# Kernel optimization log

Hardware: AMD Instinct MI355X
Metric: run time of the kernel (lower is better)

## Reference

```python
import jax, jax.numpy as jnp
import numpy as np

B, D, H = 131072, 1024, 128
ALL_PERMS = jnp.array([[0, 1, 2], [0, 2, 1], [1, 0, 2],
                       [1, 2, 0], [2, 0, 1], [2, 1, 0]], dtype=jnp.int32)


def setup_inputs() -> dict:
    key = jax.random.key(0)
    ks = jax.random.split(key, 10)
    inp_dim = D + 12  # d_model + 9 (state) + 3 (round one-hot)
    seq_embed = jax.random.normal(ks[0], (B, D), jnp.float32)
    freq = jax.random.uniform(ks[1], (B, 3), jnp.float32)
    pres = (jax.random.uniform(ks[2], (B, 3)) < 0.5).astype(jnp.float32)
    round_mask = (jax.random.uniform(ks[3], (B, 3)) < 0.5).astype(jnp.float32)
    perm_idx = jax.random.randint(ks[4], (B,), 0, 6, jnp.int32)
    W1 = jax.random.normal(ks[5], (inp_dim, H), jnp.float32) / np.sqrt(inp_dim).astype(np.float32)
    b1 = jnp.zeros((H,), jnp.float32)
    W2 = jax.random.normal(ks[6], (H, H), jnp.float32) / np.sqrt(H).astype(np.float32)
    b2 = jnp.zeros((H,), jnp.float32)
    W3 = jax.random.normal(ks[7], (H, 2), jnp.float32) / np.sqrt(H).astype(np.float32)
    b3 = jnp.zeros((2,), jnp.float32)
    return {"seq_embed": seq_embed, "freq": freq, "pres": pres,
            "round_mask": round_mask, "perm_idx": perm_idx,
            "W1": W1, "b1": b1, "W2": W2, "b2": b2, "W3": W3, "b3": b3}


def reference(seq_embed, freq, pres, round_mask, perm_idx, W1, b1, W2, b2, W3, b3):
    b = seq_embed.shape[0]
    dt = seq_embed.dtype
    perms = ALL_PERMS[perm_idx]                      # [B,3] round order per sample
    state = jnp.zeros((b, 9), dt)                    # 3 slots x [freq, pres, decoded]
    dec_f = jnp.zeros((b, 3), dt)
    dec_p = jnp.zeros((b, 3), dt)
    loss_sum = jnp.zeros((), dt)
    n_masked = jnp.zeros((), dt)
    ones_b = jnp.ones((b,), dt)
    for step in range(3):                            # fixed 3-step unroll (as original)
        ridx = perms[:, step]                        # [B]
        oh = jax.nn.one_hot(ridx, 3, dtype=dt)       # [B,3]
        gt_f = jnp.sum(freq * oh, axis=1)            # gather via one-hot
        gt_p = jnp.sum(pres * oh, axis=1)
        m = jnp.sum(round_mask * oh, axis=1)
        inp = jnp.concatenate([seq_embed, state, oh], axis=1)  # [B, D+12]
        h = jax.nn.gelu(inp @ W1 + b1, approximate=False)
        h = jax.nn.gelu(h @ W2 + b2, approximate=False)
        pred = h @ W3 + b3                           # [B,2]
        pf, z = pred[:, 0], pred[:, 1]
        fl = jnp.square(pf - gt_f) * m
        # sigmoid_cross_entropy_with_logits, numerically stable
        pl = (jnp.maximum(z, 0.0) - z * gt_p + jnp.log1p(jnp.exp(-jnp.abs(z)))) * m
        loss_sum = loss_sum + jnp.sum(fl + pl)
        n_masked = n_masked + jnp.sum(m)
        act_f = jnp.where(m > 0.5, pf, gt_f)
        act_p = jnp.where(m > 0.5, jax.nn.sigmoid(z), gt_p)
        new_vals = jnp.stack([act_f, act_p, ones_b], axis=1)   # [B,3]
        # scatter new_vals into slot ridx of state
        state3 = state.reshape(b, 3, 3)
        state = (state3 * (1.0 - oh)[:, :, None]
                 + new_vals[:, None, :] * oh[:, :, None]).reshape(b, 9)
        dec_f = dec_f * (1.0 - oh) + act_f[:, None] * oh
        dec_p = dec_p * (1.0 - oh) + act_p[:, None] * oh
    autoreg_loss = loss_sum / (n_masked + 1e-8)
    return autoreg_loss, dec_f, dec_p
```

## Files before the change

### kernel.cpp

```cpp
#include <hip/hip_runtime.h>
#include <math.h>

#define DDIM 1024
#define HDIM 128
#define BK 32

typedef float  f32x4  __attribute__((ext_vector_type(4)));
typedef __bf16 bf16x8 __attribute__((ext_vector_type(8)));

union BF2U { __bf16 h; ushort u; };

__constant__ int c_perms[6][3] = {{0,1,2},{0,2,1},{1,0,2},{1,2,0},{2,0,1},{2,1,0}};

__device__ __forceinline__ ushort f2bf(float f){
    BF2U c; c.h = (__bf16)f; return c.u;
}
__device__ __forceinline__ float gelu_fast(float x){
    float a = fabsf(x) * 0.70710678118654752f;
    float t = __frcp_rn(fmaf(0.3275911f, a, 1.0f));
    float p = t * fmaf(t, fmaf(t, fmaf(t, fmaf(t, 1.061405429f, -1.453152027f),
                 1.421413741f), -0.284496736f), 0.254829592f);
    float y = 1.0f - p * __expf(-a * a);
    float er = copysignf(y, x);
    return 0.5f * x * (1.0f + er);
}

__global__ __launch_bounds__(256) void k0_prep(const float* __restrict__ W1,
                                               const float* __restrict__ W2,
                                               ushort* __restrict__ w1s,
                                               ushort* __restrict__ w2t)
{
    int i = blockIdx.x * 256 + threadIdx.x;
    if (i < DDIM * HDIM) {
        int t = i >> 12, rem = i & 4095;
        int n = rem >> 5, kk = rem & 31;
        int k = t * 32 + kk;
        w1s[i] = f2bf(W1[(size_t)k * HDIM + n]);
    } else if (i < DDIM * HDIM + HDIM * HDIM) {
        int j = i - DDIM * HDIM;
        int k = j >> 7, n = j & 127;
        ushort b = f2bf(W2[(size_t)k * HDIM + n]);
        size_t off = (size_t)n * 256 + (size_t)(((k * 2) ^ ((n & 7) << 4)));
        w2t[off >> 1] = b;
    }
}

__global__ __launch_bounds__(256, 2) void kf_fused(
    const float* __restrict__ seq,
    const ushort* __restrict__ w1s,
    const ushort* __restrict__ w2t,
    const float* __restrict__ freq,
    const float* __restrict__ pres,
    const float* __restrict__ rmask,
    const int*   __restrict__ pidx,
    const float* __restrict__ W1,
    const float* __restrict__ b1,
    const float* __restrict__ b2,
    const float* __restrict__ W3,
    const float* __restrict__ b3,
    float* __restrict__ dec_f,
    float* __restrict__ dec_p,
    float* __restrict__ partials)
{
    __shared__ __align__(16) char lds[73728];
    const int t = threadIdx.x;
    const int wid = t >> 6, lane = t & 63;
    const int g = lane >> 4, ln = lane & 15;
    const size_t row0 = (size_t)blockIdx.x * 128;

    char* const As0 = lds;
    char* const Bs0 = lds + 49152;

    const int srow = wid * 8 + (lane >> 3);
    const int scolb = ((lane & 7) * 16) ^ ((lane >> 3) << 4);
    const int sldsw = wid * 1024;
    const int blane = lane * 16;

#define STAGE(BUF, TT) do { \
    _Pragma("unroll") \
    for (int j_ = 0; j_ < 4; ++j_) { \
        const char* ga_ = (const char*)(seq + (row0 + j_ * 32 + srow) * DDIM + (TT) * BK) + scolb; \
        char* la_ = As0 + (BUF) * 16384 + j_ * 4096 + sldsw; \
        __builtin_amdgcn_global_load_lds((const __attribute__((address_space(1))) void*)ga_, \
                                         (__attribute__((address_space(3))) void*)la_, 16, 0, 0); \
    } \
    _Pragma("unroll") \
    for (int i_ = 0; i_ < 2; ++i_) { \
        const char* gb_ = (const char*)w1s + (size_t)(TT) * 8192 + i_ * 4096 + sldsw + blane; \
        char* lb_ = Bs0 + (BUF) * 8192 + i_ * 4096 + sldsw; \
        __builtin_amdgcn_global_load_lds((const __attribute__((address_space(1))) void*)gb_, \
                                         (__attribute__((address_space(3))) void*)lb_, 16, 0, 0); \
    } } while (0)

#define COMPUTE(BUF) do { \
    bf16x8 af[2]; \
    _Pragma("unroll") \
    for (int mf = 0; mf < 2; ++mf) { \
        const int row = wid * 32 + mf * 16 + ln; \
        const int sw = (row & 7) << 4; \
        f32x4 x0 = *reinterpret_cast<const f32x4*>(As0 + (BUF) * 16384 + row * 128 + ((g * 32 +  0) ^ sw)); \
        f32x4 x1 = *reinterpret_cast<const f32x4*>(As0 + (BUF) * 16384 + row * 128 + ((g * 32 + 16) ^ sw)); \
        af[mf][0] = (__bf16)x0[0]; af[mf][1] = (__bf16)x0[1]; \
        af[mf][2] = (__bf16)x0[2]; af[mf][3] = (__bf16)x0[3]; \
        af[mf][4] = (__bf16)x1[0]; af[mf][5] = (__bf16)x1[1]; \
        af[mf][6] = (__bf16)x1[2]; af[mf][7] = (__bf16)x1[3]; \
    } \
    const ushort* btile = reinterpret_cast<const ushort*>(Bs0 + (BUF) * 8192); \
    _Pragma("unroll") \
    for (int nf = 0; nf < 8; ++nf) { \
        bf16x8 bb = *reinterpret_cast<const bf16x8*>(btile + nf * 512 + ln * 32 + g * 8); \
        acc[0][nf] = __builtin_amdgcn_mfma_f32_16x16x32_bf16(af[0], bb, acc[0][nf], 0, 0, 0); \
        acc[1][nf] = __builtin_amdgcn_mfma_f32_16x16x32_bf16(af[1], bb, acc[1][nf], 0, 0, 0); \
    } } while (0)

#define WAITBAR(N) do { \
    asm volatile("s_waitcnt vmcnt(" #N ")" ::: "memory"); \
    __builtin_amdgcn_sched_barrier(0); \
    __builtin_amdgcn_s_barrier(); \
    __builtin_amdgcn_sched_barrier(0); } while (0)

    f32x4 acc[2][8];
#pragma unroll
    for (int m = 0; m < 2; ++m)
#pragma unroll
        for (int n = 0; n < 8; ++n) acc[m][n] = (f32x4){0.f, 0.f, 0.f, 0.f};

    STAGE(0, 0);
    STAGE(1, 1);
    int cur = 0, nxt2 = 2;
    for (int tt = 0; tt < 30; ++tt) {
        WAITBAR(6);
        STAGE(nxt2, tt + 2);
        COMPUTE(cur);
        cur  = (cur  == 2) ? 0 : cur  + 1;
        nxt2 = (nxt2 == 2) ? 0 : nxt2 + 1;
    }
    WAITBAR(6);
    COMPUTE(cur);
    cur = (cur == 2) ? 0 : cur + 1;
    WAITBAR(0);
    COMPUTE(cur);
#undef WAITBAR
#undef COMPUTE
#undef STAGE

    __syncthreads();

    {
        float b1v[8];
#pragma unroll
        for (int nf = 0; nf < 8; ++nf) b1v[nf] = b1[nf * 16 + ln];
#pragma unroll
        for (int mf = 0; mf < 2; ++mf)
#pragma unroll
            for (int nf = 0; nf < 8; ++nf)
#pragma unroll
                for (int r = 0; r < 4; ++r) {
                    int row = wid * 32 + mf * 16 + g * 4 + r;
                    int colb = (nf * 32 + ln * 2) ^ ((row & 7) << 4);
                    *reinterpret_cast<ushort*>(lds + row * 256 + colb) = f2bf(acc[mf][nf][r] + b1v[nf]);
                }
    }
#pragma unroll
    for (int i = 0; i < 8; ++i) {
        const char* gs = (const char*)w2t + wid * 8192 + i * 1024 + blane;
        char* ds = lds + 32768 + wid * 8192 + i * 1024;
        __builtin_amdgcn_global_load_lds((const __attribute__((address_space(1))) void*)gs,
                                         (__attribute__((address_space(3))) void*)ds, 16, 0, 0);
    }
    {
        float* W1es = (float*)(lds + 65536);
        for (int i = t; i < 12 * 128; i += 256)
            W1es[i] = W1[(size_t)(DDIM + (i >> 7)) * HDIM + (i & 127)];
    }
    __syncthreads();

    const char*  W2s  = lds + 32768;
    const float* W1es = (const float*)(lds + 65536);
    float* stl  = (float*)(lds + 71680);
    float* redl = (float*)(lds + 72192);

    float b2v[8], w30[8], w31[8];
#pragma unroll
    for (int nf = 0; nf < 8; ++nf) {
        b2v[nf] = b2[nf * 16 + ln];
        w30[nf] = W3[(nf * 16 + ln) * 2 + 0];
        w31[nf] = W3[(nf * 16 + ln) * 2 + 1];
    }
    const float b30 = b3[0], b31 = b3[1];
    const bool owner = (ln < 4);
    float lossAcc = 0.f, maskAcc = 0.f;

    for (int p = 0; p < 2; ++p) {
        const int rowLocal = wid * 16 + ln;
        const int ctRow = p * 64 + rowLocal;
        const size_t R_h = row0 + ctRow;
        const int pidx_h = pidx[R_h];

        float scon[32];
        {
            const int swzr = (rowLocal & 7) << 4;
#pragma unroll
            for (int ks = 0; ks < 4; ++ks) {
                bf16x8 v = *reinterpret_cast<const bf16x8*>(lds + ctRow * 256 + ((ks * 64 + g * 16) ^ swzr));
#pragma unroll
                for (int j = 0; j < 8; ++j) scon[ks * 8 + j] = (float)v[j];
            }
        }
        const int rloc_own = wid * 16 + g * 4 + ln;
        const size_t R_own = row0 + (size_t)p * 64 + rloc_own;
        int pio = 0;
        float ffo[3] = {0,0,0}, ppo[3] = {0,0,0}, mmo[3] = {0,0,0};
        if (owner) {
            pio = pidx[R_own];
#pragma unroll
            for (int q = 0; q < 3; ++q) {
                ffo[q] = freq[R_own * 3 + q];
                ppo[q] = pres[R_own * 3 + q];
                mmo[q] = rmask[R_own * 3 + q];
            }
        }

        for (int s = 0; s < 3; ++s) {
            const int ridx_h = c_perms[pidx_h][s];
            bf16x8 afr[4];
#pragma unroll
            for (int ks = 0; ks < 4; ++ks) {
                const float* ohp = &W1es[(9 + ridx_h) * 128 + ks * 32 + g * 8];
                f32x4 o0 = *reinterpret_cast<const f32x4*>(ohp);
                f32x4 o1 = *reinterpret_cast<const f32x4*>(ohp + 4);
#pragma unroll
                for (int j = 0; j < 4; ++j) {
                    afr[ks][j]     = (__bf16)gelu_fast(scon[ks * 8 + j]     + o0[j]);
                    afr[ks][4 + j] = (__bf16)gelu_fast(scon[ks * 8 + 4 + j] + o1[j]);
                }
            }
            f32x4 acc2[8];
#pragma unroll
            for (int nf = 0; nf < 8; ++nf) acc2[nf] = (f32x4){0.f, 0.f, 0.f, 0.f};
#pragma unroll
            for (int ks = 0; ks < 4; ++ks) {
#pragma unroll
                for (int nf = 0; nf < 8; ++nf) {
                    const int n = nf * 16 + ln;
                    bf16x8 bb = *reinterpret_cast<const bf16x8*>(W2s + n * 256 + ((ks * 64 + g * 16) ^ ((n & 7) << 4)));
                    acc2[nf] = __builtin_amdgcn_mfma_f32_16x16x32_bf16(afr[ks], bb, acc2[nf], 0, 0, 0);
                }
            }
            float p0[4] = {0, 0, 0, 0}, p1[4] = {0, 0, 0, 0};
#pragma unroll
            for (int nf = 0; nf < 8; ++nf) {
#pragma unroll
                for (int r = 0; r < 4; ++r) {
                    float h2 = gelu_fast(acc2[nf][r] + b2v[nf]);
                    p0[r] += h2 * w30[nf];
                    p1[r] += h2 * w31[nf];
                }
            }
#pragma unroll
            for (int mk = 1; mk < 16; mk <<= 1) {
#pragma unroll
                for (int r = 0; r < 4; ++r) {
                    p0[r] += __shfl_xor(p0[r], mk);
                    p1[r] += __shfl_xor(p1[r], mk);
                }
            }
            if (owner) {
                const int ridx_o = c_perms[pio][s];
                float pf = ((ln == 0) ? p0[0] : (ln == 1) ? p0[1] : (ln == 2) ? p0[2] : p0[3]) + b30;
                float z  = ((ln == 0) ? p1[0] : (ln == 1) ? p1[1] : (ln == 2) ? p1[2] : p1[3]) + b31;
                float gt_f = (ridx_o == 0) ? ffo[0] : (ridx_o == 1) ? ffo[1] : ffo[2];
                float gt_p = (ridx_o == 0) ? ppo[0] : (ridx_o == 1) ? ppo[1] : ppo[2];
                float m    = (ridx_o == 0) ? mmo[0] : (ridx_o == 1) ? mmo[1] : mmo[2];
                float d = pf - gt_f;
                float pl = (fmaxf(z, 0.f) - z * gt_p + __logf(1.0f + __expf(-fabsf(z)))) * m;
                lossAcc += d * d * m + pl;
                maskAcc += m;
                bool msk = m > 0.5f;
                float act_f = msk ? pf : gt_f;
                float act_p = msk ? (1.f / (1.f + __expf(-z))) : gt_p;
                stl[rloc_own * 2 + 0] = act_f;
                stl[rloc_own * 2 + 1] = act_p;
                dec_f[R_own * 3 + ridx_o] = act_f;
                dec_p[R_own * 3 + ridx_o] = act_p;
            }
            if (s < 2) {
                float af = stl[rowLocal * 2 + 0];
                float ap = stl[rowLocal * 2 + 1];
                const float* w0r = &W1es[(ridx_h * 3 + 0) * 128];
                const float* w1r = &W1es[(ridx_h * 3 + 1) * 128];
                const float* w2r = &W1es[(ridx_h * 3 + 2) * 128];
#pragma unroll
                for (int ks = 0; ks < 4; ++ks) {
                    const int c0 = ks * 32 + g * 8;
                    f32x4 a0 = *reinterpret_cast<const f32x4*>(w0r + c0);
                    f32x4 a1 = *reinterpret_cast<const f32x4*>(w0r + c0 + 4);
                    f32x4 b0 = *reinterpret_cast<const f32x4*>(w1r + c0);
                    f32x4 b1x = *reinterpret_cast<const f32x4*>(w1r + c0 + 4);
                    f32x4 c0v = *reinterpret_cast<const f32x4*>(w2r + c0);
                    f32x4 c1v = *reinterpret_cast<const f32x4*>(w2r + c0 + 4);
#pragma unroll
                    for (int j = 0; j < 4; ++j) {
                        scon[ks * 8 + j]     += af * a0[j] + ap * b0[j]  + c0v[j];
                        scon[ks * 8 + 4 + j] += af * a1[j] + ap * b1x[j] + c1v[j];
                    }
                }
            }
        }
    }
#pragma unroll
    for (int mk = 1; mk < 64; mk <<= 1) {
        lossAcc += __shfl_xor(lossAcc, mk);
        maskAcc += __shfl_xor(maskAcc, mk);
    }
    if (lane == 0) { redl[wid * 2] = lossAcc; redl[wid * 2 + 1] = maskAcc; }
    __syncthreads();
    if (t == 0) {
        float ls = 0.f, ms = 0.f;
#pragma unroll
        for (int w = 0; w < 4; ++w) { ls += redl[w * 2]; ms += redl[w * 2 + 1]; }
        partials[2 * (size_t)blockIdx.x]     = ls;
        partials[2 * (size_t)blockIdx.x + 1] = ms;
    }
}

__global__ __launch_bounds__(256) void k3_reduce(const float* __restrict__ partials,
                                                 int nb, float* __restrict__ out)
{
    __shared__ float sl[256], sm[256];
    int t = threadIdx.x;
    float ls = 0.f, ms = 0.f;
    for (int i = t; i < nb; i += 256) { ls += partials[2 * i]; ms += partials[2 * i + 1]; }
    sl[t] = ls; sm[t] = ms;
    __syncthreads();
    for (int s = 128; s > 0; s >>= 1) {
        if (t < s) { sl[t] += sl[t + s]; sm[t] += sm[t + s]; }
        __syncthreads();
    }
    if (t == 0) out[0] = sl[0] / (sm[0] + 1e-8f);
}

extern "C" void kernel_launch(void* const* d_in, const int* in_sizes, int n_in,
                              void* d_out, int out_size, void* d_ws, size_t ws_size,
                              hipStream_t stream) {
    const float* seq   = (const float*)d_in[0];
    const float* freq  = (const float*)d_in[1];
    const float* pres  = (const float*)d_in[2];
    const float* rmask = (const float*)d_in[3];
    const int*   pidx  = (const int*)d_in[4];
    const float* W1    = (const float*)d_in[5];
    const float* b1    = (const float*)d_in[6];
    const float* W2    = (const float*)d_in[7];
    const float* b2    = (const float*)d_in[8];
    const float* W3    = (const float*)d_in[9];
    const float* b3    = (const float*)d_in[10];

    int B = in_sizes[4];
    float* out   = (float*)d_out;
    float* dec_f = out + 1;
    float* dec_p = out + 1 + (size_t)B * 3;

    char* ws = (char*)d_ws;
    float*  partials = (float*)ws;
    ushort* w1s  = (ushort*)(ws + 16384);
    ushort* w2t  = (ushort*)(ws + 16384 + 262144);

    int nblk = B / 128;
    k0_prep<<<(DDIM * HDIM + HDIM * HDIM + 255) / 256, 256, 0, stream>>>(W1, W2, w1s, w2t);
    kf_fused<<<nblk, 256, 0, stream>>>(seq, w1s, w2t, freq, pres, rmask, pidx,
                                       W1, b1, b2, W3, b3, dec_f, dec_p, partials);
    k3_reduce<<<1, 256, 0, stream>>>(partials, nblk, out);
}
```

Measured before the change: 202.4 us.

## Make each wave own its rows and drop block barriers from the GEMM loop

Restructures the fused MLP kernel so each wave stages and processes its own 32 rows in a private LDS arena, removing the per-iteration block barrier from the layer-1 K loop. W1 tiles now go directly from global memory into registers, triple-buffered across iterations, instead of through LDS. W2 is preloaded into LDS once at kernel start. The small W1 extra rows are read from global memory rather than copied into LDS. This raises register pressure and global reads of W1 per wave, and the LDS footprint grows.

```diff
diff --git a/kernel.cpp b/kernel.cpp
--- a/kernel.cpp
+++ b/kernel.cpp
@@ -3,7 +3,6 @@
 
 #define DDIM 1024
 #define HDIM 128
-#define BK 32
 
 typedef float  f32x4  __attribute__((ext_vector_type(4)));
 typedef __bf16 bf16x8 __attribute__((ext_vector_type(8)));
@@ -62,61 +61,64 @@
     float* __restrict__ dec_p,
     float* __restrict__ partials)
 {
-    __shared__ __align__(16) char lds[73728];
+    __shared__ __align__(16) char lds[81920];
     const int t = threadIdx.x;
     const int wid = t >> 6, lane = t & 63;
     const int g = lane >> 4, ln = lane & 15;
-    const size_t row0 = (size_t)blockIdx.x * 128;
-
-    char* const As0 = lds;
-    char* const Bs0 = lds + 49152;
-
-    const int srow = wid * 8 + (lane >> 3);
+    const size_t gr0 = (size_t)blockIdx.x * 128 + wid * 32;
+
+#pragma unroll
+    for (int i = 0; i < 8; ++i) {
+        const char* gs = (const char*)w2t + wid * 1024 + i * 4096 + lane * 16;
+        char* ds = lds + wid * 1024 + i * 4096;
+        __builtin_amdgcn_global_load_lds((const __attribute__((address_space(1))) void*)gs,
+                                         (__attribute__((address_space(3))) void*)ds, 16, 0, 0);
+    }
+    asm volatile("s_waitcnt vmcnt(0)" ::: "memory");
+    __syncthreads();
+
+    char* const arena = lds + 32768 + wid * 12288;
+    const int srow  = lane >> 3;
     const int scolb = ((lane & 7) * 16) ^ ((lane >> 3) << 4);
-    const int sldsw = wid * 1024;
-    const int blane = lane * 16;
-
-#define STAGE(BUF, TT) do { \
+    const int boff  = ln * 64 + g * 16;
+
+#define STAGEA(BUF, TT) do { \
     _Pragma("unroll") \
     for (int j_ = 0; j_ < 4; ++j_) { \
-        const char* ga_ = (const char*)(seq + (row0 + j_ * 32 + srow) * DDIM + (TT) * BK) + scolb; \
-        char* la_ = As0 + (BUF) * 16384 + j_ * 4096 + sldsw; \
+        const char* ga_ = (const char*)(seq + (gr0 + j_ * 8 + srow) * DDIM) + (TT) * 128 + scolb; \
+        char* la_ = arena + (BUF) * 4096 + j_ * 1024; \
         __builtin_amdgcn_global_load_lds((const __attribute__((address_space(1))) void*)ga_, \
                                          (__attribute__((address_space(3))) void*)la_, 16, 0, 0); \
+    } } while (0)
+
+#define LOADB(ARR, TT) do { \
+    const char* bp_ = (const char*)w1s + (size_t)(TT) * 8192 + boff; \
+    _Pragma("unroll") \
+    for (int nf_ = 0; nf_ < 8; ++nf_) \
+        ARR[nf_] = *reinterpret_cast<const bf16x8*>(bp_ + nf_ * 1024); \
+    } while (0)
+
+#define COMPUTE(BUF, ARR) do { \
+    bf16x8 af[2]; \
+    const int sw_ = (ln & 7) << 4; \
+    _Pragma("unroll") \
+    for (int mf_ = 0; mf_ < 2; ++mf_) { \
+        const int p_ = mf_ * 16 + ln; \
+        f32x4 x0 = *reinterpret_cast<const f32x4*>(arena + (BUF) * 4096 + p_ * 128 + ((g * 32 +  0) ^ sw_)); \
+        f32x4 x1 = *reinterpret_cast<const f32x4*>(arena + (BUF) * 4096 + p_ * 128 + ((g * 32 + 16) ^ sw_)); \
+        af[mf_][0] = (__bf16)x0[0]; af[mf_][1] = (__bf16)x0[1]; \
+        af[mf_][2] = (__bf16)x0[2]; af[mf_][3] = (__bf16)x0[3]; \
+        af[mf_][4] = (__bf16)x1[0]; af[mf_][5] = (__bf16)x1[1]; \
+        af[mf_][6] = (__bf16)x1[2]; af[mf_][7] = (__bf16)x1[3]; \
     } \
     _Pragma("unroll") \
-    for (int i_ = 0; i_ < 2; ++i_) { \
-        const char* gb_ = (const char*)w1s + (size_t)(TT) * 8192 + i_ * 4096 + sldsw + blane; \
-        char* lb_ = Bs0 + (BUF) * 8192 + i_ * 4096 + sldsw; \
-        __builtin_amdgcn_global_load_lds((const __attribute__((address_space(1))) void*)gb_, \
-                                         (__attribute__((address_space(3))) void*)lb_, 16, 0, 0); \
+    for (int nf_ = 0; nf_ < 8; ++nf_) { \
+        acc[0][nf_] = __builtin_amdgcn_mfma_f32_16x16x32_bf16(af[0], ARR[nf_], acc[0][nf_], 0, 0, 0); \
+        acc[1][nf_] = __builtin_amdgcn_mfma_f32_16x16x32_bf16(af[1], ARR[nf_], acc[1][nf_], 0, 0, 0); \
     } } while (0)
 
-#define COMPUTE(BUF) do { \
-    bf16x8 af[2]; \
-    _Pragma("unroll") \
-    for (int mf = 0; mf < 2; ++mf) { \
-        const int row = wid * 32 + mf * 16 + ln; \
-        const int sw = (row & 7) << 4; \
-        f32x4 x0 = *reinterpret_cast<const f32x4*>(As0 + (BUF) * 16384 + row * 128 + ((g * 32 +  0) ^ sw)); \
-        f32x4 x1 = *reinterpret_cast<const f32x4*>(As0 + (BUF) * 16384 + row * 128 + ((g * 32 + 16) ^ sw)); \
-        af[mf][0] = (__bf16)x0[0]; af[mf][1] = (__bf16)x0[1]; \
-        af[mf][2] = (__bf16)x0[2]; af[mf][3] = (__bf16)x0[3]; \
-        af[mf][4] = (__bf16)x1[0]; af[mf][5] = (__bf16)x1[1]; \
-        af[mf][6] = (__bf16)x1[2]; af[mf][7] = (__bf16)x1[3]; \
-    } \
-    const ushort* btile = reinterpret_cast<const ushort*>(Bs0 + (BUF) * 8192); \
-    _Pragma("unroll") \
-    for (int nf = 0; nf < 8; ++nf) { \
-        bf16x8 bb = *reinterpret_cast<const bf16x8*>(btile + nf * 512 + ln * 32 + g * 8); \
-        acc[0][nf] = __builtin_amdgcn_mfma_f32_16x16x32_bf16(af[0], bb, acc[0][nf], 0, 0, 0); \
-        acc[1][nf] = __builtin_amdgcn_mfma_f32_16x16x32_bf16(af[1], bb, acc[1][nf], 0, 0, 0); \
-    } } while (0)
-
-#define WAITBAR(N) do { \
+#define WAITV(N) do { \
     asm volatile("s_waitcnt vmcnt(" #N ")" ::: "memory"); \
-    __builtin_amdgcn_sched_barrier(0); \
-    __builtin_amdgcn_s_barrier(); \
     __builtin_amdgcn_sched_barrier(0); } while (0)
 
     f32x4 acc[2][8];
@@ -125,26 +127,22 @@
 #pragma unroll
         for (int n = 0; n < 8; ++n) acc[m][n] = (f32x4){0.f, 0.f, 0.f, 0.f};
 
-    STAGE(0, 0);
-    STAGE(1, 1);
-    int cur = 0, nxt2 = 2;
-    for (int tt = 0; tt < 30; ++tt) {
-        WAITBAR(6);
-        STAGE(nxt2, tt + 2);
-        COMPUTE(cur);
-        cur  = (cur  == 2) ? 0 : cur  + 1;
-        nxt2 = (nxt2 == 2) ? 0 : nxt2 + 1;
-    }
-    WAITBAR(6);
-    COMPUTE(cur);
-    cur = (cur == 2) ? 0 : cur + 1;
-    WAITBAR(0);
-    COMPUTE(cur);
-#undef WAITBAR
+    bf16x8 bA[8], bB[8], bC[8];
+    LOADB(bA, 0); STAGEA(0, 0);
+    LOADB(bB, 1); STAGEA(1, 1);
+
+    for (int tt = 0; tt < 30; tt += 3) {
+        WAITV(12); LOADB(bC, tt + 2); STAGEA(2, tt + 2); COMPUTE(0, bA);
+        WAITV(12); LOADB(bA, tt + 3); STAGEA(0, tt + 3); COMPUTE(1, bB);
+        WAITV(12); LOADB(bB, tt + 4); STAGEA(1, tt + 4); COMPUTE(2, bC);
+    }
+    WAITV(12); COMPUTE(0, bA);
+    WAITV(0);  COMPUTE(1, bB);
+
+#undef WAITV
 #undef COMPUTE
-#undef STAGE
-
-    __syncthreads();
+#undef LOADB
+#undef STAGEA
 
     {
         float b1v[8];
@@ -156,29 +154,15 @@
             for (int nf = 0; nf < 8; ++nf)
 #pragma unroll
                 for (int r = 0; r < 4; ++r) {
-                    int row = wid * 32 + mf * 16 + g * 4 + r;
-                    int colb = (nf * 32 + ln * 2) ^ ((row & 7) << 4);
-                    *reinterpret_cast<ushort*>(lds + row * 256 + colb) = f2bf(acc[mf][nf][r] + b1v[nf]);
-                }
-    }
-#pragma unroll
-    for (int i = 0; i < 8; ++i) {
-        const char* gs = (const char*)w2t + wid * 8192 + i * 1024 + blane;
-        char* ds = lds + 32768 + wid * 8192 + i * 1024;
-        __builtin_amdgcn_global_load_lds((const __attribute__((address_space(1))) void*)gs,
-                                         (__attribute__((address_space(3))) void*)ds, 16, 0, 0);
-    }
-    {
-        float* W1es = (float*)(lds + 65536);
-        for (int i = t; i < 12 * 128; i += 256)
-            W1es[i] = W1[(size_t)(DDIM + (i >> 7)) * HDIM + (i & 127)];
-    }
-    __syncthreads();
-
-    const char*  W2s  = lds + 32768;
-    const float* W1es = (const float*)(lds + 65536);
-    float* stl  = (float*)(lds + 71680);
-    float* redl = (float*)(lds + 72192);
+                    int p = mf * 16 + g * 4 + r;
+                    int colb = (nf * 32 + ln * 2) ^ ((p & 7) << 4);
+                    *reinterpret_cast<ushort*>(arena + p * 256 + colb) = f2bf(acc[mf][nf][r] + b1v[nf]);
+                }
+    }
+
+    const char* W2s = lds;
+    float* stl   = (float*)(arena + 8192);
+    float* lossw = (float*)(arena + 8448);
 
     float b2v[8], w30[8], w31[8];
 #pragma unroll
@@ -191,33 +175,32 @@
     const bool owner = (ln < 4);
     float lossAcc = 0.f, maskAcc = 0.f;
 
-    for (int p = 0; p < 2; ++p) {
-        const int rowLocal = wid * 16 + ln;
-        const int ctRow = p * 64 + rowLocal;
-        const size_t R_h = row0 + ctRow;
+    for (int q = 0; q < 2; ++q) {
+        const int prow = q * 16 + ln;
+        const size_t R_h = gr0 + prow;
         const int pidx_h = pidx[R_h];
 
         float scon[32];
         {
-            const int swzr = (rowLocal & 7) << 4;
+            const int swzr = (ln & 7) << 4;
 #pragma unroll
             for (int ks = 0; ks < 4; ++ks) {
-                bf16x8 v = *reinterpret_cast<const bf16x8*>(lds + ctRow * 256 + ((ks * 64 + g * 16) ^ swzr));
+                bf16x8 v = *reinterpret_cast<const bf16x8*>(arena + prow * 256 + ((ks * 64 + g * 16) ^ swzr));
 #pragma unroll
                 for (int j = 0; j < 8; ++j) scon[ks * 8 + j] = (float)v[j];
             }
         }
-        const int rloc_own = wid * 16 + g * 4 + ln;
-        const size_t R_own = row0 + (size_t)p * 64 + rloc_own;
+        const int rloc = g * 4 + ln;
+        const size_t R_own = gr0 + q * 16 + rloc;
         int pio = 0;
         float ffo[3] = {0,0,0}, ppo[3] = {0,0,0}, mmo[3] = {0,0,0};
         if (owner) {
             pio = pidx[R_own];
 #pragma unroll
-            for (int q = 0; q < 3; ++q) {
-                ffo[q] = freq[R_own * 3 + q];
-                ppo[q] = pres[R_own * 3 + q];
-                mmo[q] = rmask[R_own * 3 + q];
+            for (int qq = 0; qq < 3; ++qq) {
+                ffo[qq] = freq[R_own * 3 + qq];
+                ppo[qq] = pres[R_own * 3 + qq];
+                mmo[qq] = rmask[R_own * 3 + qq];
             }
         }
 
@@ -226,7 +209,7 @@
             bf16x8 afr[4];
 #pragma unroll
             for (int ks = 0; ks < 4; ++ks) {
-                const float* ohp = &W1es[(9 + ridx_h) * 128 + ks * 32 + g * 8];
+                const float* ohp = &W1[(size_t)(DDIM + 9 + ridx_h) * HDIM + ks * 32 + g * 8];
                 f32x4 o0 = *reinterpret_cast<const f32x4*>(ohp);
                 f32x4 o1 = *reinterpret_cast<const f32x4*>(ohp + 4);
 #pragma unroll
@@ -279,17 +262,17 @@
                 bool msk = m > 0.5f;
                 float act_f = msk ? pf : gt_f;
                 float act_p = msk ? (1.f / (1.f + __expf(-z))) : gt_p;
-                stl[rloc_own * 2 + 0] = act_f;
-                stl[rloc_own * 2 + 1] = act_p;
+                stl[rloc * 2 + 0] = act_f;
+                stl[rloc * 2 + 1] = act_p;
                 dec_f[R_own * 3 + ridx_o] = act_f;
                 dec_p[R_own * 3 + ridx_o] = act_p;
             }
             if (s < 2) {
-                float af = stl[rowLocal * 2 + 0];
-                float ap = stl[rowLocal * 2 + 1];
-                const float* w0r = &W1es[(ridx_h * 3 + 0) * 128];
-                const float* w1r = &W1es[(ridx_h * 3 + 1) * 128];
-                const float* w2r = &W1es[(ridx_h * 3 + 2) * 128];
+                float af_ = stl[ln * 2 + 0];
+                float ap_ = stl[ln * 2 + 1];
+                const float* w0r = &W1[(size_t)(DDIM + ridx_h * 3 + 0) * HDIM];
+                const float* w1r = &W1[(size_t)(DDIM + ridx_h * 3 + 1) * HDIM];
+                const float* w2r = &W1[(size_t)(DDIM + ridx_h * 3 + 2) * HDIM];
 #pragma unroll
                 for (int ks = 0; ks < 4; ++ks) {
                     const int c0 = ks * 32 + g * 8;
@@ -301,8 +284,8 @@
                     f32x4 c1v = *reinterpret_cast<const f32x4*>(w2r + c0 + 4);
 #pragma unroll
                     for (int j = 0; j < 4; ++j) {
-                        scon[ks * 8 + j]     += af * a0[j] + ap * b0[j]  + c0v[j];
-                        scon[ks * 8 + 4 + j] += af * a1[j] + ap * b1x[j] + c1v[j];
+                        scon[ks * 8 + j]     += af_ * a0[j] + ap_ * b0[j]  + c0v[j];
+                        scon[ks * 8 + 4 + j] += af_ * a1[j] + ap_ * b1x[j] + c1v[j];
                     }
                 }
             }
@@ -313,12 +296,15 @@
         lossAcc += __shfl_xor(lossAcc, mk);
         maskAcc += __shfl_xor(maskAcc, mk);
     }
-    if (lane == 0) { redl[wid * 2] = lossAcc; redl[wid * 2 + 1] = maskAcc; }
+    if (lane == 0) { lossw[0] = lossAcc; lossw[1] = maskAcc; }
     __syncthreads();
     if (t == 0) {
         float ls = 0.f, ms = 0.f;
 #pragma unroll
-        for (int w = 0; w < 4; ++w) { ls += redl[w * 2]; ms += redl[w * 2 + 1]; }
+        for (int w = 0; w < 4; ++w) {
+            const float* lw = (const float*)(lds + 32768 + w * 12288 + 8448);
+            ls += lw[0]; ms += lw[1];
+        }
         partials[2 * (size_t)blockIdx.x]     = ls;
         partials[2 * (size_t)blockIdx.x + 1] = ms;
     }
```

Measured after the change: 231.6 us. 14.4% more time.

## Halve block row tile to 64 and read W2 from global to raise occupancy

Applied to the files above, without the earlier changes.

Each block now processes 64 rows instead of 128, with one M-fragment per wave. LDS drops from 72KB to 48KB because the W2 tile is no longer staged in shared memory and is read directly from global/L2 in the second layer. Launch bounds move to 3 blocks per CU so more blocks can be resident and hide memory latency. In exchange, W1 tile traffic per row doubles (each W1 tile serves half as many rows), and the W2 reads now go through the cache instead of LDS.

```diff
diff --git a/kernel.cpp b/kernel.cpp
--- a/kernel.cpp
+++ b/kernel.cpp
@@ -3,7 +3,6 @@
 
 #define DDIM 1024
 #define HDIM 128
-#define BK 32
 
 typedef float  f32x4  __attribute__((ext_vector_type(4)));
 typedef __bf16 bf16x8 __attribute__((ext_vector_type(8)));
@@ -45,7 +44,7 @@
     }
 }
 
-__global__ __launch_bounds__(256, 2) void kf_fused(
+__global__ __launch_bounds__(256, 3) void kf_fused(
     const float* __restrict__ seq,
     const ushort* __restrict__ w1s,
     const ushort* __restrict__ w2t,
@@ -62,55 +61,50 @@
     float* __restrict__ dec_p,
     float* __restrict__ partials)
 {
-    __shared__ __align__(16) char lds[73728];
+    __shared__ __align__(16) char lds[49152];
     const int t = threadIdx.x;
     const int wid = t >> 6, lane = t & 63;
     const int g = lane >> 4, ln = lane & 15;
-    const size_t row0 = (size_t)blockIdx.x * 128;
-
-    char* const As0 = lds;
-    char* const Bs0 = lds + 49152;
-
-    const int srow = wid * 8 + (lane >> 3);
+    const size_t row0 = (size_t)blockIdx.x * 64;
+
+    const int srow  = wid * 8 + (lane >> 3);
     const int scolb = ((lane & 7) * 16) ^ ((lane >> 3) << 4);
     const int sldsw = wid * 1024;
     const int blane = lane * 16;
 
 #define STAGE(BUF, TT) do { \
     _Pragma("unroll") \
-    for (int j_ = 0; j_ < 4; ++j_) { \
-        const char* ga_ = (const char*)(seq + (row0 + j_ * 32 + srow) * DDIM + (TT) * BK) + scolb; \
-        char* la_ = As0 + (BUF) * 16384 + j_ * 4096 + sldsw; \
+    for (int j_ = 0; j_ < 2; ++j_) { \
+        const char* ga_ = (const char*)(seq + (row0 + j_ * 32 + srow) * DDIM + (TT) * 32) + scolb; \
+        char* la_ = lds + (BUF) * 8192 + j_ * 4096 + sldsw; \
         __builtin_amdgcn_global_load_lds((const __attribute__((address_space(1))) void*)ga_, \
                                          (__attribute__((address_space(3))) void*)la_, 16, 0, 0); \
     } \
     _Pragma("unroll") \
     for (int i_ = 0; i_ < 2; ++i_) { \
         const char* gb_ = (const char*)w1s + (size_t)(TT) * 8192 + i_ * 4096 + sldsw + blane; \
-        char* lb_ = Bs0 + (BUF) * 8192 + i_ * 4096 + sldsw; \
+        char* lb_ = lds + 24576 + (BUF) * 8192 + i_ * 4096 + sldsw; \
         __builtin_amdgcn_global_load_lds((const __attribute__((address_space(1))) void*)gb_, \
                                          (__attribute__((address_space(3))) void*)lb_, 16, 0, 0); \
     } } while (0)
 
 #define COMPUTE(BUF) do { \
-    bf16x8 af[2]; \
+    bf16x8 af; \
+    { \
+        const int p_ = wid * 16 + ln; \
+        const int sw_ = (p_ & 7) << 4; \
+        f32x4 x0 = *reinterpret_cast<const f32x4*>(lds + (BUF) * 8192 + p_ * 128 + ((g * 32 +  0) ^ sw_)); \
+        f32x4 x1 = *reinterpret_cast<const f32x4*>(lds + (BUF) * 8192 + p_ * 128 + ((g * 32 + 16) ^ sw_)); \
+        af[0] = (__bf16)x0[0]; af[1] = (__bf16)x0[1]; \
+        af[2] = (__bf16)x0[2]; af[3] = (__bf16)x0[3]; \
+        af[4] = (__bf16)x1[0]; af[5] = (__bf16)x1[1]; \
+        af[6] = (__bf16)x1[2]; af[7] = (__bf16)x1[3]; \
+    } \
+    const ushort* btile = reinterpret_cast<const ushort*>(lds + 24576 + (BUF) * 8192); \
     _Pragma("unroll") \
-    for (int mf = 0; mf < 2; ++mf) { \
-        const int row = wid * 32 + mf * 16 + ln; \
-        const int sw = (row & 7) << 4; \
-        f32x4 x0 = *reinterpret_cast<const f32x4*>(As0 + (BUF) * 16384 + row * 128 + ((g * 32 +  0) ^ sw)); \
-        f32x4 x1 = *reinterpret_cast<const f32x4*>(As0 + (BUF) * 16384 + row * 128 + ((g * 32 + 16) ^ sw)); \
-        af[mf][0] = (__bf16)x0[0]; af[mf][1] = (__bf16)x0[1]; \
-        af[mf][2] = (__bf16)x0[2]; af[mf][3] = (__bf16)x0[3]; \
-        af[mf][4] = (__bf16)x1[0]; af[mf][5] = (__bf16)x1[1]; \
-        af[mf][6] = (__bf16)x1[2]; af[mf][7] = (__bf16)x1[3]; \
-    } \
-    const ushort* btile = reinterpret_cast<const ushort*>(Bs0 + (BUF) * 8192); \
-    _Pragma("unroll") \
-    for (int nf = 0; nf < 8; ++nf) { \
-        bf16x8 bb = *reinterpret_cast<const bf16x8*>(btile + nf * 512 + ln * 32 + g * 8); \
-        acc[0][nf] = __builtin_amdgcn_mfma_f32_16x16x32_bf16(af[0], bb, acc[0][nf], 0, 0, 0); \
-        acc[1][nf] = __builtin_amdgcn_mfma_f32_16x16x32_bf16(af[1], bb, acc[1][nf], 0, 0, 0); \
+    for (int nf_ = 0; nf_ < 8; ++nf_) { \
+        bf16x8 bb = *reinterpret_cast<const bf16x8*>(btile + nf_ * 512 + ln * 32 + g * 8); \
+        acc[nf_] = __builtin_amdgcn_mfma_f32_16x16x32_bf16(af, bb, acc[nf_], 0, 0, 0); \
     } } while (0)
 
 #define WAITBAR(N) do { \
@@ -119,23 +113,21 @@
     __builtin_amdgcn_s_barrier(); \
     __builtin_amdgcn_sched_barrier(0); } while (0)
 
-    f32x4 acc[2][8];
-#pragma unroll
-    for (int m = 0; m < 2; ++m)
-#pragma unroll
-        for (int n = 0; n < 8; ++n) acc[m][n] = (f32x4){0.f, 0.f, 0.f, 0.f};
+    f32x4 acc[8];
+#pragma unroll
+    for (int n = 0; n < 8; ++n) acc[n] = (f32x4){0.f, 0.f, 0.f, 0.f};
 
     STAGE(0, 0);
     STAGE(1, 1);
     int cur = 0, nxt2 = 2;
     for (int tt = 0; tt < 30; ++tt) {
-        WAITBAR(6);
+        WAITBAR(4);
         STAGE(nxt2, tt + 2);
         COMPUTE(cur);
         cur  = (cur  == 2) ? 0 : cur  + 1;
         nxt2 = (nxt2 == 2) ? 0 : nxt2 + 1;
     }
-    WAITBAR(6);
+    WAITBAR(4);
     COMPUTE(cur);
     cur = (cur == 2) ? 0 : cur + 1;
     WAITBAR(0);
@@ -151,34 +143,24 @@
 #pragma unroll
         for (int nf = 0; nf < 8; ++nf) b1v[nf] = b1[nf * 16 + ln];
 #pragma unroll
-        for (int mf = 0; mf < 2; ++mf)
-#pragma unroll
-            for (int nf = 0; nf < 8; ++nf)
-#pragma unroll
-                for (int r = 0; r < 4; ++r) {
-                    int row = wid * 32 + mf * 16 + g * 4 + r;
-                    int colb = (nf * 32 + ln * 2) ^ ((row & 7) << 4);
-                    *reinterpret_cast<ushort*>(lds + row * 256 + colb) = f2bf(acc[mf][nf][r] + b1v[nf]);
-                }
-    }
-#pragma unroll
-    for (int i = 0; i < 8; ++i) {
-        const char* gs = (const char*)w2t + wid * 8192 + i * 1024 + blane;
-        char* ds = lds + 32768 + wid * 8192 + i * 1024;
-        __builtin_amdgcn_global_load_lds((const __attribute__((address_space(1))) void*)gs,
-                                         (__attribute__((address_space(3))) void*)ds, 16, 0, 0);
+        for (int nf = 0; nf < 8; ++nf)
+#pragma unroll
+            for (int r = 0; r < 4; ++r) {
+                int row = wid * 16 + g * 4 + r;
+                int colb = (nf * 32 + ln * 2) ^ ((row & 7) << 4);
+                *reinterpret_cast<ushort*>(lds + row * 256 + colb) = f2bf(acc[nf][r] + b1v[nf]);
+            }
     }
     {
-        float* W1es = (float*)(lds + 65536);
+        float* W1es = (float*)(lds + 24576);
         for (int i = t; i < 12 * 128; i += 256)
             W1es[i] = W1[(size_t)(DDIM + (i >> 7)) * HDIM + (i & 127)];
     }
     __syncthreads();
 
-    const char*  W2s  = lds + 32768;
-    const float* W1es = (const float*)(lds + 65536);
-    float* stl  = (float*)(lds + 71680);
-    float* redl = (float*)(lds + 72192);
+    const float* W1es = (const float*)(lds + 24576);
+    float* stl   = (float*)(lds + 30720 + wid * 128);
+    float* lossw = (float*)(lds + 31232 + wid * 8);
 
     float b2v[8], w30[8], w31[8];
 #pragma unroll
@@ -191,24 +173,23 @@
     const bool owner = (ln < 4);
     float lossAcc = 0.f, maskAcc = 0.f;
 
-    for (int p = 0; p < 2; ++p) {
-        const int rowLocal = wid * 16 + ln;
-        const int ctRow = p * 64 + rowLocal;
-        const size_t R_h = row0 + ctRow;
+    {
+        const int prow = wid * 16 + ln;
+        const size_t R_h = row0 + prow;
         const int pidx_h = pidx[R_h];
 
         float scon[32];
         {
-            const int swzr = (rowLocal & 7) << 4;
+            const int swzr = (ln & 7) << 4;
 #pragma unroll
             for (int ks = 0; ks < 4; ++ks) {
-                bf16x8 v = *reinterpret_cast<const bf16x8*>(lds + ctRow * 256 + ((ks * 64 + g * 16) ^ swzr));
+                bf16x8 v = *reinterpret_cast<const bf16x8*>(lds + prow * 256 + ((ks * 64 + g * 16) ^ swzr));
 #pragma unroll
                 for (int j = 0; j < 8; ++j) scon[ks * 8 + j] = (float)v[j];
             }
         }
-        const int rloc_own = wid * 16 + g * 4 + ln;
-        const size_t R_own = row0 + (size_t)p * 64 + rloc_own;
+        const int rloc = g * 4 + ln;
+        const size_t R_own = row0 + wid * 16 + rloc;
         int pio = 0;
         float ffo[3] = {0,0,0}, ppo[3] = {0,0,0}, mmo[3] = {0,0,0};
         if (owner) {
@@ -243,7 +224,8 @@
 #pragma unroll
                 for (int nf = 0; nf < 8; ++nf) {
                     const int n = nf * 16 + ln;
-                    bf16x8 bb = *reinterpret_cast<const bf16x8*>(W2s + n * 256 + ((ks * 64 + g * 16) ^ ((n & 7) << 4)));
+                    bf16x8 bb = *reinterpret_cast<const bf16x8*>(
+                        (const char*)w2t + n * 256 + ((ks * 64 + g * 16) ^ ((n & 7) << 4)));
                     acc2[nf] = __builtin_amdgcn_mfma_f32_16x16x32_bf16(afr[ks], bb, acc2[nf], 0, 0, 0);
                 }
             }
@@ -279,14 +261,14 @@
                 bool msk = m > 0.5f;
                 float act_f = msk ? pf : gt_f;
                 float act_p = msk ? (1.f / (1.f + __expf(-z))) : gt_p;
-                stl[rloc_own * 2 + 0] = act_f;
-                stl[rloc_own * 2 + 1] = act_p;
+                stl[rloc * 2 + 0] = act_f;
+                stl[rloc * 2 + 1] = act_p;
                 dec_f[R_own * 3 + ridx_o] = act_f;
                 dec_p[R_own * 3 + ridx_o] = act_p;
             }
             if (s < 2) {
-                float af = stl[rowLocal * 2 + 0];
-                float ap = stl[rowLocal * 2 + 1];
+                float af_ = stl[ln * 2 + 0];
+                float ap_ = stl[ln * 2 + 1];
                 const float* w0r = &W1es[(ridx_h * 3 + 0) * 128];
                 const float* w1r = &W1es[(ridx_h * 3 + 1) * 128];
                 const float* w2r = &W1es[(ridx_h * 3 + 2) * 128];
@@ -301,8 +283,8 @@
                     f32x4 c1v = *reinterpret_cast<const f32x4*>(w2r + c0 + 4);
 #pragma unroll
                     for (int j = 0; j < 4; ++j) {
-                        scon[ks * 8 + j]     += af * a0[j] + ap * b0[j]  + c0v[j];
-                        scon[ks * 8 + 4 + j] += af * a1[j] + ap * b1x[j] + c1v[j];
+                        scon[ks * 8 + j]     += af_ * a0[j] + ap_ * b0[j]  + c0v[j];
+                        scon[ks * 8 + 4 + j] += af_ * a1[j] + ap_ * b1x[j] + c1v[j];
                     }
                 }
             }
@@ -313,12 +295,15 @@
         lossAcc += __shfl_xor(lossAcc, mk);
         maskAcc += __shfl_xor(maskAcc, mk);
     }
-    if (lane == 0) { redl[wid * 2] = lossAcc; redl[wid * 2 + 1] = maskAcc; }
+    if (lane == 0) { lossw[0] = lossAcc; lossw[1] = maskAcc; }
     __syncthreads();
     if (t == 0) {
         float ls = 0.f, ms = 0.f;
 #pragma unroll
-        for (int w = 0; w < 4; ++w) { ls += redl[w * 2]; ms += redl[w * 2 + 1]; }
+        for (int w = 0; w < 4; ++w) {
+            const float* lw = (const float*)(lds + 31232 + w * 8);
+            ls += lw[0]; ms += lw[1];
+        }
         partials[2 * (size_t)blockIdx.x]     = ls;
         partials[2 * (size_t)blockIdx.x + 1] = ms;
     }
@@ -365,7 +350,7 @@
     ushort* w1s  = (ushort*)(ws + 16384);
     ushort* w2t  = (ushort*)(ws + 16384 + 262144);
 
-    int nblk = B / 128;
+    int nblk = B / 64;
     k0_prep<<<(DDIM * HDIM + HDIM * HDIM + 255) / 256, 256, 0, stream>>>(W1, W2, w1s, w2t);
     kf_fused<<<nblk, 256, 0, stream>>>(seq, w1s, w2t, freq, pres, rmask, pidx,
                                        W1, b1, b2, W3, b3, dec_f, dec_p, partials);
```

Result: slower. 361.5 us (+78.6%).
